# Kernel tuning notes

Hardware: AMD Instinct MI355X
Metric: run time of the kernel (lower is better)

The kernel has to match this reference:

```python
import math
import jax, jax.numpy as jnp
import numpy as np

D_MODEL = 1024
N_HEADS = 16
HEAD_DIM = D_MODEL // N_HEADS  # 64
QDIM = HEAD_DIM // 4           # 16
SPIKE_SLOPE = 5.0
B, S = 2, 2048


def _qweight(r, i, j, k):
    # Hamilton-product weight matrix, identical to QLinear.forward's torch.cat construction.
    return jnp.concatenate([
        jnp.concatenate([r, -i, -j, -k], 1),
        jnp.concatenate([i, r, -k, j], 1),
        jnp.concatenate([j, k, r, -i], 1),
        jnp.concatenate([k, -j, i, r], 1),
    ], 0)


def setup_inputs() -> dict:
    key = jax.random.key(0)
    ks = jax.random.split(key, 20)
    Qo = Qi = D_MODEL // 4  # 256
    p = lambda k, shape, s=0.02: (jax.random.normal(k, shape, dtype=jnp.float32) * s)
    inp = {
        'query': jax.random.normal(ks[0], (B, S, D_MODEL), dtype=jnp.float32),
        'key_in': jax.random.normal(ks[1], (B, S, D_MODEL), dtype=jnp.float32),
        'value': jax.random.normal(ks[2], (B, S, D_MODEL), dtype=jnp.float32),
        'mask': jnp.ones((B, S), dtype=jnp.int32),
        'density_feat': jax.random.normal(ks[3], (B, S, 3), dtype=jnp.float32),
        # q_proj QLinear params
        'wq_r': p(ks[4], (Qo, Qi)), 'wq_i': p(ks[5], (Qo, Qi)),
        'wq_j': p(ks[6], (Qo, Qi)), 'wq_k': p(ks[7], (Qo, Qi)),
        'bq': jnp.zeros((D_MODEL,), jnp.float32),
        # k_proj QLinear params
        'wk_r': p(ks[8], (Qo, Qi)), 'wk_i': p(ks[9], (Qo, Qi)),
        'wk_j': p(ks[10], (Qo, Qi)), 'wk_k': p(ks[11], (Qo, Qi)),
        'bk': jnp.zeros((D_MODEL,), jnp.float32),
        # v_proj / out_proj dense params
        'wv': p(ks[12], (D_MODEL, D_MODEL)), 'bv': jnp.zeros((D_MODEL,), jnp.float32),
        'wo': p(ks[13], (D_MODEL, D_MODEL)), 'bo': jnp.zeros((D_MODEL,), jnp.float32),
        # learned spike threshold (init -1.0 as in torch)
        'threshold': jnp.asarray(-1.0, dtype=jnp.float32),
        # density_mod MLP (use nonzero values so the gate shift is exercised)
        'dm1_w': p(ks[14], (16, 3), 0.5), 'dm1_b': p(ks[15], (16,), 0.1),
        'dm2_w': p(ks[16], (1, 16), 0.5), 'dm2_b': p(ks[17], (1,), 0.1),
    }
    return inp


def reference(query, key_in, value, mask, density_feat,
              wq_r, wq_i, wq_j, wq_k, bq,
              wk_r, wk_i, wk_j, wk_k, bk,
              wv, bv, wo, bo, threshold,
              dm1_w, dm1_b, dm2_w, dm2_b):
    H, hd, Qd = N_HEADS, HEAD_DIM, QDIM
    Bq, Sq, D = query.shape

    Wq = _qweight(wq_r, wq_i, wq_j, wq_k)
    Wk = _qweight(wk_r, wk_i, wk_j, wk_k)
    q = query @ Wq.T + bq
    k = key_in @ Wk.T + bk
    v = value @ wv.T + bv

    # head-major split, matching torch.cat(x.split(hd, -1), dim=0)
    qh = q.reshape(Bq, Sq, H, hd).transpose(2, 0, 1, 3)  # (H,B,S,hd)
    kh = k.reshape(Bq, Sq, H, hd).transpose(2, 0, 1, 3)
    vh = v.reshape(Bq, Sq, H, hd).transpose(2, 0, 1, 3)

    # sum of 4 quaternion-component dot products == full dot product over hd
    scores = jnp.einsum('hbmd,hbnd->hbmn', qh, kh) / math.sqrt(Qd)
    scores = jnp.clip(scores, -6.0, 6.0)

    base_threshold = jax.nn.softplus(threshold)
    h1 = jax.nn.gelu(density_feat @ dm1_w.T + dm1_b, approximate=False)
    d_shift = (h1 @ dm2_w.T + dm2_b)[..., 0]  # (B,N)
    thr = base_threshold + d_shift[None, :, None, :] * 0.1  # (1,B,1,N)

    spike_gate = jax.nn.sigmoid(SPIKE_SLOPE * (scores - thr))
    mod = scores * (1.0 + spike_gate * 2.0)

    m2 = (mask[:, :, None] * mask[:, None, :])[None]  # (1,B,N,N)
    mod = jnp.where(m2 == 0, -10000.0, mod)

    weights = jax.nn.softmax(jnp.clip(mod, -30.0, 30.0), axis=-1)
    # dropout: eval mode (identity)
    out_h = jnp.einsum('hbmn,hbnd->hbmd', weights, vh)
    out = out_h.transpose(1, 2, 0, 3).reshape(Bq, Sq, D)
    return out @ wo.T + bo
```

## Files before the change

kernel.cpp:

```cpp
#include <hip/hip_runtime.h>
#include <stdint.h>
#include <math.h>

#define BB 2
#define SS 2048
#define DM 1024
#define NH 16
#define HD 64
#define MTOT (BB*SS)

typedef __bf16 bf16x8 __attribute__((ext_vector_type(8)));
typedef float  f32x4  __attribute__((ext_vector_type(4)));
typedef float  f32x2  __attribute__((ext_vector_type(2)));
typedef uint32_t u32x4 __attribute__((ext_vector_type(4)));

__device__ __forceinline__ unsigned short f2bf(float f) {
  __bf16 h = (__bf16)f;
  return __builtin_bit_cast(unsigned short, h);
}

__device__ __forceinline__ bf16x8 ldsv8(const unsigned short* p) {
  return __builtin_bit_cast(bf16x8, *(const u32x4*)p);
}

__device__ __forceinline__ void gl16(const void* g, void* l) {
  __builtin_amdgcn_global_load_lds(
      (const __attribute__((address_space(1))) uint32_t*)g,
      (__attribute__((address_space(3))) uint32_t*)l, 16, 0, 0);
}

#define MFMA16(a,b,c) __builtin_amdgcn_mfma_f32_16x16x32_bf16((a),(b),(c),0,0,0)

#define C_NEG5L2E  (-7.213475204444817f)
#define C_L2E      (1.4426950408889634f)
#define C_18L2E    (25.968510736001341f)

__device__ __forceinline__ f32x2 gate_pk(f32x2 s2, float kth, f32x2& lr) {
  s2 = __builtin_elementwise_min(__builtin_elementwise_max(s2, (f32x2){-6.f,-6.f}), (f32x2){6.f,6.f});
  const f32x2 targ = __builtin_elementwise_fma(s2, (f32x2){C_NEG5L2E, C_NEG5L2E}, (f32x2){kth, kth});
  f32x2 t;
  t.x = __builtin_amdgcn_exp2f(targ.x);
  t.y = __builtin_amdgcn_exp2f(targ.y);
  const f32x2 den = t + (f32x2){1.f, 1.f};
  f32x2 g;
  g.x = __builtin_amdgcn_rcpf(den.x);
  g.y = __builtin_amdgcn_rcpf(den.y);
  const f32x2 md = __builtin_elementwise_fma(s2 + s2, g, s2);
  const f32x2 pa = __builtin_elementwise_fma(md, (f32x2){C_L2E, C_L2E}, (f32x2){-C_18L2E, -C_18L2E});
  f32x2 p;
  p.x = __builtin_amdgcn_exp2f(pa.x);
  p.y = __builtin_amdgcn_exp2f(pa.y);
  lr += p;
  return p;
}

__global__ __launch_bounds__(256) void prep_all(
    const float* __restrict__ wqr, const float* __restrict__ wqi,
    const float* __restrict__ wqj, const float* __restrict__ wqk,
    const float* __restrict__ wkr, const float* __restrict__ wki,
    const float* __restrict__ wkj, const float* __restrict__ wkk,
    const float* __restrict__ wv,  const float* __restrict__ wo,
    unsigned short* __restrict__ Wq, unsigned short* __restrict__ Wk,
    unsigned short* __restrict__ Wv, unsigned short* __restrict__ Wo,
    const float* __restrict__ query, const float* __restrict__ key_in,
    const float* __restrict__ value,
    unsigned short* __restrict__ qcv, unsigned short* __restrict__ kcv,
    unsigned short* __restrict__ vcv,
    const float* __restrict__ density, const float* __restrict__ dm1w,
    const float* __restrict__ dm1b, const float* __restrict__ dm2w,
    const float* __restrict__ dm2b, const float* __restrict__ thr_s,
    const int* __restrict__ mask, float2* __restrict__ klim,
    int* __restrict__ amask)
{
  const int bid = blockIdx.x;
  if (bid < 512) {
    const int idx = (bid * 256 + threadIdx.x) * 8;
    const int o = idx >> 10, i = idx & 1023;
    const int br = o >> 8, bc = i >> 8;
    const int ro = o & 255, ci = i & 255;
    const int comp[4][4] = {{0,1,2,3},{1,0,3,2},{2,3,0,1},{3,2,1,0}};
    const float sgn[4][4] = {{1.f,-1.f,-1.f,-1.f},{1.f,1.f,-1.f,1.f},{1.f,1.f,1.f,-1.f},{1.f,-1.f,1.f,1.f}};
    const float* pq[4] = {wqr, wqi, wqj, wqk};
    const float* pk[4] = {wkr, wki, wkj, wkk};
    const int c_ = comp[br][bc];
    const float s_ = sgn[br][bc];
    const float* qsrc = pq[c_] + ro * 256 + ci;
    const float* ksrc = pk[c_] + ro * 256 + ci;
    {
      const float4 f0 = *(const float4*)qsrc;
      const float4 f1 = *(const float4*)(qsrc + 4);
      union { unsigned short us[8]; u32x4 v; } t;
      t.us[0]=f2bf(s_*f0.x); t.us[1]=f2bf(s_*f0.y); t.us[2]=f2bf(s_*f0.z); t.us[3]=f2bf(s_*f0.w);
      t.us[4]=f2bf(s_*f1.x); t.us[5]=f2bf(s_*f1.y); t.us[6]=f2bf(s_*f1.z); t.us[7]=f2bf(s_*f1.w);
      *(u32x4*)(Wq + idx) = t.v;
    }
    {
      const float4 f0 = *(const float4*)ksrc;
      const float4 f1 = *(const float4*)(ksrc + 4);
      union { unsigned short us[8]; u32x4 v; } t;
      t.us[0]=f2bf(s_*f0.x); t.us[1]=f2bf(s_*f0.y); t.us[2]=f2bf(s_*f0.z); t.us[3]=f2bf(s_*f0.w);
      t.us[4]=f2bf(s_*f1.x); t.us[5]=f2bf(s_*f1.y); t.us[6]=f2bf(s_*f1.z); t.us[7]=f2bf(s_*f1.w);
      *(u32x4*)(Wk + idx) = t.v;
    }
    {
      const float4 f0 = *(const float4*)(wv + idx);
      const float4 f1 = *(const float4*)(wv + idx + 4);
      union { unsigned short us[8]; u32x4 v; } t;
      t.us[0]=f2bf(f0.x); t.us[1]=f2bf(f0.y); t.us[2]=f2bf(f0.z); t.us[3]=f2bf(f0.w);
      t.us[4]=f2bf(f1.x); t.us[5]=f2bf(f1.y); t.us[6]=f2bf(f1.z); t.us[7]=f2bf(f1.w);
      *(u32x4*)(Wv + idx) = t.v;
    }
    {
      const float4 f0 = *(const float4*)(wo + idx);
      const float4 f1 = *(const float4*)(wo + idx + 4);
      union { unsigned short us[8]; u32x4 v; } t;
      t.us[0]=f2bf(f0.x); t.us[1]=f2bf(f0.y); t.us[2]=f2bf(f0.z); t.us[3]=f2bf(f0.w);
      t.us[4]=f2bf(f1.x); t.us[5]=f2bf(f1.y); t.us[6]=f2bf(f1.z); t.us[7]=f2bf(f1.w);
      *(u32x4*)(Wo + idx) = t.v;
    }
  } else if (bid < 2560) {
    const int i8 = ((bid - 512) * 256 + threadIdx.x) * 8;
    {
      const float4 f0 = *(const float4*)(query + i8);
      const float4 f1 = *(const float4*)(query + i8 + 4);
      union { unsigned short us[8]; u32x4 v; } t;
      t.us[0]=f2bf(f0.x); t.us[1]=f2bf(f0.y); t.us[2]=f2bf(f0.z); t.us[3]=f2bf(f0.w);
      t.us[4]=f2bf(f1.x); t.us[5]=f2bf(f1.y); t.us[6]=f2bf(f1.z); t.us[7]=f2bf(f1.w);
      *(u32x4*)(qcv + i8) = t.v;
    }
    {
      const float4 f0 = *(const float4*)(key_in + i8);
      const float4 f1 = *(const float4*)(key_in + i8 + 4);
      union { unsigned short us[8]; u32x4 v; } t;
      t.us[0]=f2bf(f0.x); t.us[1]=f2bf(f0.y); t.us[2]=f2bf(f0.z); t.us[3]=f2bf(f0.w);
      t.us[4]=f2bf(f1.x); t.us[5]=f2bf(f1.y); t.us[6]=f2bf(f1.z); t.us[7]=f2bf(f1.w);
      *(u32x4*)(kcv + i8) = t.v;
    }
    {
      const float4 f0 = *(const float4*)(value + i8);
      const float4 f1 = *(const float4*)(value + i8 + 4);
      union { unsigned short us[8]; u32x4 v; } t;
      t.us[0]=f2bf(f0.x); t.us[1]=f2bf(f0.y); t.us[2]=f2bf(f0.z); t.us[3]=f2bf(f0.w);
      t.us[4]=f2bf(f1.x); t.us[5]=f2bf(f1.y); t.us[6]=f2bf(f1.z); t.us[7]=f2bf(f1.w);
      *(u32x4*)(vcv + i8) = t.v;
    }
  } else {
    const int i = (bid - 2560) * 256 + threadIdx.x;
    if (i >= BB * SS) return;
    const float x0 = density[i*3+0], x1 = density[i*3+1], x2 = density[i*3+2];
    const float base = log1pf(expf(thr_s[0]));
    float acc = dm2b[0];
    #pragma unroll
    for (int j = 0; j < 16; ++j) {
      const float hj = dm1w[j*3+0]*x0 + dm1w[j*3+1]*x1 + dm1w[j*3+2]*x2 + dm1b[j];
      const float ge = 0.5f * hj * (1.0f + erff(hj * 0.70710678118654752f));
      acc += dm2w[j] * ge;
    }
    const float thr = base + 0.1f * acc;
    const int mk = mask[i];
    klim[i] = make_float2(thr * (-C_NEG5L2E),
                          mk ? 1e30f : -30.0f);
    const unsigned long long any = __ballot(mk == 0);
    if ((threadIdx.x & 63) == 0 && any)
      atomicOr(&amask[i >> 11], 1);
  }
}

struct GemmArgs {
  const unsigned short* A[3];
  const unsigned short* W[3];
  const float* bias[3];
  void* out[3];
  float scale[3];
  int omode[3];
};

template<int DB>
__global__ __launch_bounds__(256) void gemm_bt(GemmArgs args)
{
  __shared__ __align__(16) unsigned short lA[DB + 1][128*64];
  __shared__ __align__(16) unsigned short lB[DB + 1][128*64];
  const int z = blockIdx.y;
  const int tid = threadIdx.x;
  const int wid = tid >> 6, lane = tid & 63;
  const int l15 = lane & 15, l4 = lane >> 4;
  const int bm = blockIdx.x & 31, bn = blockIdx.x >> 5;
  const int row0 = bm * 128, col0 = bn * 128;
  const int wm = (wid >> 1) * 64, wn = (wid & 1) * 64;

  const unsigned short* gA[4];
  const unsigned short* gB[4];
  #pragma unroll
  for (int i = 0; i < 4; ++i) {
    const int c = (wid * 4 + i) * 64 + lane;
    const int r = c >> 3, jx = c & 7, j = jx ^ (r & 7);
    gA[i] = args.A[z] + (row0 + r) * 1024 + j * 8;
    gB[i] = args.W[z] + (col0 + r) * 1024 + j * 8;
  }

  f32x4 acc[4][4];
  #pragma unroll
  for (int i = 0; i < 4; ++i)
    #pragma unroll
    for (int j = 0; j < 4; ++j) acc[i][j] = (f32x4){0.f,0.f,0.f,0.f};

  #pragma unroll
  for (int i = 0; i < 4; ++i) {
    gl16(gA[i], &lA[0][(wid * 4 + i) * 512]);
    gl16(gB[i], &lB[0][(wid * 4 + i) * 512]);
  }
  if (DB) __syncthreads();

  for (int kt = 0; kt < 16; ++kt) {
    const int cb = DB ? (kt & 1) : 0;
    if (DB) {
      if (kt < 15) {
        const int nb = cb ^ 1, k0 = (kt + 1) * 64;
        #pragma unroll
        for (int i = 0; i < 4; ++i) {
          gl16(gA[i] + k0, &lA[nb][(wid * 4 + i) * 512]);
          gl16(gB[i] + k0, &lB[nb][(wid * 4 + i) * 512]);
        }
      }
    } else {
      if (kt > 0) {
        const int k0 = kt * 64;
        #pragma unroll
        for (int i = 0; i < 4; ++i) {
          gl16(gA[i] + k0, &lA[0][(wid * 4 + i) * 512]);
          gl16(gB[i] + k0, &lB[0][(wid * 4 + i) * 512]);
        }
      }
      __syncthreads();
    }
    #pragma unroll
    for (int kk = 0; kk < 2; ++kk) {
      const int kl = kk * 32 + l4 * 8;
      bf16x8 af[4], bfb[4];
      #pragma unroll
      for (int mi = 0; mi < 4; ++mi) {
        const int r = wm + mi * 16 + l15;
        af[mi] = ldsv8(&lA[cb][r * 64 + (kl ^ ((r & 7) << 3))]);
      }
      #pragma unroll
      for (int nj = 0; nj < 4; ++nj) {
        const int r = wn + nj * 16 + l15;
        bfb[nj] = ldsv8(&lB[cb][r * 64 + (kl ^ ((r & 7) << 3))]);
      }
      #pragma unroll
      for (int mi = 0; mi < 4; ++mi)
        #pragma unroll
        for (int nj = 0; nj < 4; ++nj)
          acc[mi][nj] = MFMA16(af[mi], bfb[nj], acc[mi][nj]);
    }
    __syncthreads();
  }

  const int om = args.omode[z];
  const float sc = args.scale[z];
  void* Cptr = args.out[z];
  #pragma unroll
  for (int nj = 0; nj < 4; ++nj) {
    const int c = col0 + wn + nj * 16 + l15;
    const float bv_ = args.bias[z][c];
    #pragma unroll
    for (int mi = 0; mi < 4; ++mi) {
      const int rb = row0 + wm + mi * 16 + l4 * 4;
      #pragma unroll
      for (int e = 0; e < 4; ++e) {
        const float val = (acc[mi][nj][e] + bv_) * sc;
        const int r = rb + e;
        if (om == 0) {
          ((unsigned short*)Cptr)[r * 1024 + c] = f2bf(val);
        } else if (om == 2) {
          ((float*)Cptr)[r * 1024 + c] = val;
        } else {
          const int h = c >> 6, d = c & 63, b = r >> 11, s = r & 2047;
          ((unsigned short*)Cptr)[((h * BB + b) * HD + d) * SS + s] = f2bf(val);
        }
      }
    }
  }
}

__global__ __launch_bounds__(256, 4) void attn_kernel(
    const unsigned short* __restrict__ qg, const unsigned short* __restrict__ kg,
    const unsigned short* __restrict__ vT, const float2* __restrict__ klim,
    const int* __restrict__ mask, const int* __restrict__ amask,
    unsigned short* __restrict__ outg)
{
  __shared__ __align__(16) unsigned short smem[20480];
  unsigned char* sb = (unsigned char*)smem;
  unsigned short* lK = smem;
  unsigned short* lV = smem + 8192;
  unsigned short* lP = smem + 16384;

  const int tid = threadIdx.x;
  const int wid = tid >> 6, lane = tid & 63;
  const int l15 = lane & 15, l4 = lane >> 4;
  const int rg = wid >> 1, par = wid & 1;
  const int hb = blockIdx.x & 31, qb = blockIdx.x >> 5;
  const int h = hb >> 1, b = hb & 1;
  const int qr0 = qb * 64 + rg * 32;

  const unsigned short* kbase = kg + (b * SS) * DM + h * HD;
  const unsigned short* vbase = vT + ((h * BB + b) * HD) * SS;
  const float2* klimb = klim + b * SS;
  const int clean = (amask[b] == 0);

  const int krho = wid * 8 + (lane >> 3);
  const int kc   = (lane & 7) ^ ((krho >> 1) & 7);
  const unsigned short* ksrc0 = kbase + (size_t)krho * DM + kc * 8;
  const unsigned short* ksrc1 = kbase + (size_t)(32 + krho) * DM + kc * 8;
  const int vd_  = wid * 16 + (lane >> 2);
  const int vc   = (lane & 3) ^ (vd_ & 3);
  const unsigned short* vsrc0 = vbase + (size_t)vd_ * SS + vc * 8;
  const unsigned short* vsrc1 = vbase + (size_t)vd_ * SS + 32 + vc * 8;
  unsigned char* kd0 = sb + wid * 1024;
  unsigned char* kd1 = sb + 4096 + wid * 1024;
  unsigned char* vd0 = sb + 16384 + wid * 1024;
  unsigned char* vd1 = sb + 16384 + 4096 + wid * 1024;

  bf16x8 aq[2][2];
  #pragma unroll
  for (int sr = 0; sr < 2; ++sr) {
    const unsigned short* qs = qg + (b * SS + qr0 + sr * 16 + l15) * DM + h * HD + l4 * 8;
    aq[sr][0] = __builtin_bit_cast(bf16x8, *(const u32x4*)qs);
    aq[sr][1] = __builtin_bit_cast(bf16x8, *(const u32x4*)(qs + 32));
  }
  float limq[2][4];
  if (!clean) {
    #pragma unroll
    for (int sr = 0; sr < 2; ++sr)
      #pragma unroll
      for (int e = 0; e < 4; ++e)
        limq[sr][e] = mask[b * SS + qr0 + sr * 16 + l4 * 4 + e] ? 1e30f : -30.0f;
  }

  f32x2 lr01[2] = {{0.f,0.f},{0.f,0.f}}, lr23[2] = {{0.f,0.f},{0.f,0.f}};
  f32x4 o[2][4];
  #pragma unroll
  for (int sr = 0; sr < 2; ++sr)
    #pragma unroll
    for (int d = 0; d < 4; ++d) o[sr][d] = (f32x4){0.f,0.f,0.f,0.f};

  unsigned short* lPw = lP + wid * 1024;

  gl16(ksrc0, kd0);
  gl16(ksrc1, kd1);
  gl16(vsrc0, vd0);
  gl16(vsrc1, vd1);
  __syncthreads();

  #pragma unroll 2
  for (int pr = 0; pr < 32; ++pr) {
    const int cur = pr & 1;
    const unsigned short* lKt = lK + cur * 4096 + par * 2048;
    const unsigned short* lVt = lV + cur * 4096 + par * 2048;
    const int n0 = pr * 64 + par * 32;

    if (pr < 31) {
      const int co = (cur ^ 1) * 8192;
      const size_t ko = (size_t)(pr + 1) * 64 * DM;
      gl16(ksrc0 + ko, kd0 + co);
      gl16(ksrc1 + ko, kd1 + co);
      gl16(vsrc0 + (pr + 1) * 64, vd0 + co);
      gl16(vsrc1 + (pr + 1) * 64, vd1 + co);
    }

    const float4 klA = *(const float4*)(klimb + n0 + 2 * l15);

    f32x4 sv[2][2];
    __builtin_amdgcn_s_setprio(1);
    #pragma unroll
    for (int cf = 0; cf < 2; ++cf) {
      const int r = 2 * l15 + cf;
      const bf16x8 kf0 = ldsv8(&lKt[r * 64 + ((l4 * 8) ^ ((l15 & 7) << 3))]);
      const bf16x8 kf1 = ldsv8(&lKt[r * 64 + ((32 + l4 * 8) ^ ((l15 & 7) << 3))]);
      #pragma unroll
      for (int sr = 0; sr < 2; ++sr) {
        f32x4 a = (f32x4){0.f,0.f,0.f,0.f};
        a = MFMA16(aq[sr][0], kf0, a);
        a = MFMA16(aq[sr][1], kf1, a);
        sv[sr][cf] = a;
      }
    }
    __builtin_amdgcn_s_setprio(0);

    f32x2 p01[2][2], p23[2][2];
    if (clean) {
      #pragma unroll
      for (int sr = 0; sr < 2; ++sr)
        #pragma unroll
        for (int cf = 0; cf < 2; ++cf) {
          const float kth = cf ? klA.z : klA.x;
          p01[sr][cf] = gate_pk((f32x2){sv[sr][cf][0], sv[sr][cf][1]}, kth, lr01[sr]);
          p23[sr][cf] = gate_pk((f32x2){sv[sr][cf][2], sv[sr][cf][3]}, kth, lr23[sr]);
        }
    } else {
      #pragma unroll
      for (int sr = 0; sr < 2; ++sr)
        #pragma unroll
        for (int cf = 0; cf < 2; ++cf) {
          const float kth = cf ? klA.z : klA.x;
          const float klm = cf ? klA.w : klA.y;
          float pe[4];
          #pragma unroll
          for (int e = 0; e < 4; ++e) {
            float s = fminf(fmaxf(sv[sr][cf][e], -6.f), 6.f);
            const float t = __builtin_amdgcn_exp2f(fmaf(s, C_NEG5L2E, kth));
            const float g = __builtin_amdgcn_rcpf(1.f + t);
            float md = fmaf(s + s, g, s);
            md = fminf(md, fminf(klm, limq[sr][e]));
            pe[e] = __builtin_amdgcn_exp2f(fmaf(md, C_L2E, -C_18L2E));
          }
          p01[sr][cf] = (f32x2){pe[0], pe[1]};
          p23[sr][cf] = (f32x2){pe[2], pe[3]};
          lr01[sr] += p01[sr][cf];
          lr23[sr] += p23[sr][cf];
        }
    }

    #pragma unroll
    for (int sr = 0; sr < 2; ++sr)
      #pragma unroll
      for (int e = 0; e < 4; ++e) {
        const int rr = l4 * 4 + e;
        const float pa_ = (e < 2) ? p01[sr][0][e] : p23[sr][0][e - 2];
        const float pb_ = (e < 2) ? p01[sr][1][e] : p23[sr][1][e - 2];
        union { unsigned short us[2]; unsigned int u; } pk2;
        pk2.us[0] = f2bf(pa_);
        pk2.us[1] = f2bf(pb_);
        *(unsigned int*)&lPw[sr * 512 + rr * 32 + ((2 * l15) ^ ((rr & 3) << 3))] = pk2.u;
      }
    asm volatile("s_waitcnt lgkmcnt(0)" ::: "memory");
    __builtin_amdgcn_sched_barrier(0);

    const bf16x8 pa0 = ldsv8(&lPw[l15 * 32 + ((l4 * 8) ^ ((l15 & 3) << 3))]);
    const bf16x8 pa1 = ldsv8(&lPw[512 + l15 * 32 + ((l4 * 8) ^ ((l15 & 3) << 3))]);

    __builtin_amdgcn_s_setprio(1);
    #pragma unroll
    for (int df = 0; df < 4; ++df) {
      const int d = df * 16 + l15;
      const bf16x8 vf = ldsv8(&lVt[d * 32 + ((l4 * 8) ^ ((d & 3) << 3))]);
      o[0][df] = MFMA16(pa0, vf, o[0][df]);
      o[1][df] = MFMA16(pa1, vf, o[1][df]);
    }
    __builtin_amdgcn_s_setprio(0);

    __syncthreads();
  }

  __syncthreads();
  float* xch = (float*)smem;
  float* slot = xch + rg * 2560;
  if (par) {
    #pragma unroll
    for (int sr = 0; sr < 2; ++sr) {
      #pragma unroll
      for (int df = 0; df < 4; ++df)
        *(f32x4*)&slot[((sr * 4 + df) * 64 + lane) * 4] = o[sr][df];
      f32x4 lr;
      lr[0] = lr01[sr].x; lr[1] = lr01[sr].y; lr[2] = lr23[sr].x; lr[3] = lr23[sr].y;
      *(f32x4*)&slot[2048 + (sr * 64 + lane) * 4] = lr;
    }
  }
  __syncthreads();
  if (!par) {
    #pragma unroll
    for (int sr = 0; sr < 2; ++sr) {
      #pragma unroll
      for (int df = 0; df < 4; ++df) {
        const f32x4 t = *(const f32x4*)&slot[((sr * 4 + df) * 64 + lane) * 4];
        o[sr][df][0] += t[0]; o[sr][df][1] += t[1]; o[sr][df][2] += t[2]; o[sr][df][3] += t[3];
      }
      const f32x4 lrq = *(const f32x4*)&slot[2048 + (sr * 64 + lane) * 4];
      const float lrun[4] = {lr01[sr].x, lr01[sr].y, lr23[sr].x, lr23[sr].y};
      #pragma unroll
      for (int e = 0; e < 4; ++e) {
        float ls = lrun[e] + lrq[e];
        ls += __shfl_xor(ls, 1);
        ls += __shfl_xor(ls, 2);
        ls += __shfl_xor(ls, 4);
        ls += __shfl_xor(ls, 8);
        const float rl = __builtin_amdgcn_rcpf(ls);
        const int r = qr0 + sr * 16 + l4 * 4 + e;
        #pragma unroll
        for (int df = 0; df < 4; ++df) {
          outg[(b * SS + r) * DM + h * HD + df * 16 + l15] = f2bf(o[sr][df][e] * rl);
        }
      }
    }
  }
}

extern "C" void kernel_launch(void* const* d_in, const int* in_sizes, int n_in,
                              void* d_out, int out_size, void* d_ws, size_t ws_size,
                              hipStream_t stream)
{
  const float* query   = (const float*)d_in[0];
  const float* key_in  = (const float*)d_in[1];
  const float* value   = (const float*)d_in[2];
  const int*   mask    = (const int*)d_in[3];
  const float* density = (const float*)d_in[4];
  const float* wq_r = (const float*)d_in[5];
  const float* wq_i = (const float*)d_in[6];
  const float* wq_j = (const float*)d_in[7];
  const float* wq_k = (const float*)d_in[8];
  const float* bq   = (const float*)d_in[9];
  const float* wk_r = (const float*)d_in[10];
  const float* wk_i = (const float*)d_in[11];
  const float* wk_j = (const float*)d_in[12];
  const float* wk_k = (const float*)d_in[13];
  const float* bk   = (const float*)d_in[14];
  const float* wv   = (const float*)d_in[15];
  const float* bv   = (const float*)d_in[16];
  const float* wo   = (const float*)d_in[17];
  const float* bo   = (const float*)d_in[18];
  const float* thrs = (const float*)d_in[19];
  const float* dm1w = (const float*)d_in[20];
  const float* dm1b = (const float*)d_in[21];
  const float* dm2w = (const float*)d_in[22];
  const float* dm2b = (const float*)d_in[23];

  char* ws = (char*)d_ws;
  unsigned short* Wq  = (unsigned short*)(ws + ((size_t)0 << 20));
  unsigned short* Wk  = (unsigned short*)(ws + ((size_t)2 << 20));
  unsigned short* Wv  = (unsigned short*)(ws + ((size_t)4 << 20));
  unsigned short* Wo  = (unsigned short*)(ws + ((size_t)6 << 20));
  unsigned short* qbf = (unsigned short*)(ws + ((size_t)8 << 20));
  unsigned short* kbf = (unsigned short*)(ws + ((size_t)16 << 20));
  unsigned short* vT  = (unsigned short*)(ws + ((size_t)24 << 20));
  unsigned short* att = (unsigned short*)(ws + ((size_t)32 << 20));
  float2* klim        = (float2*)(ws + ((size_t)40 << 20));
  int* amask          = (int*)(ws + ((size_t)40 << 20) + 65536);

  unsigned short* qcv = (unsigned short*)d_out;
  unsigned short* kcv = (unsigned short*)d_out + (size_t)MTOT * DM;
  unsigned short* vcv = att;

  hipMemsetAsync(amask, 0, 2 * sizeof(int), stream);
  prep_all<<<2576, 256, 0, stream>>>(
      wq_r, wq_i, wq_j, wq_k, wk_r, wk_i, wk_j, wk_k, wv, wo,
      Wq, Wk, Wv, Wo,
      query, key_in, value, qcv, kcv, vcv,
      density, dm1w, dm1b, dm2w, dm2b, thrs, mask, klim, amask);

  GemmArgs qkv;
  qkv.A[0] = qcv; qkv.W[0] = Wq; qkv.bias[0] = bq; qkv.out[0] = qbf; qkv.scale[0] = 0.25f; qkv.omode[0] = 0;
  qkv.A[1] = kcv; qkv.W[1] = Wk; qkv.bias[1] = bk; qkv.out[1] = kbf; qkv.scale[1] = 1.0f;  qkv.omode[1] = 0;
  qkv.A[2] = vcv; qkv.W[2] = Wv; qkv.bias[2] = bv; qkv.out[2] = vT;  qkv.scale[2] = 1.0f;  qkv.omode[2] = 1;
  gemm_bt<0><<<dim3(256, 3), 256, 0, stream>>>(qkv);

  attn_kernel<<<1024, 256, 0, stream>>>(qbf, kbf, vT, klim, mask, amask, att);

  GemmArgs og;
  og.A[0] = att; og.W[0] = Wo; og.bias[0] = bo; og.out[0] = d_out; og.scale[0] = 1.0f; og.omode[0] = 2;
  og.A[1] = att; og.W[1] = Wo; og.bias[1] = bo; og.out[1] = d_out; og.scale[1] = 1.0f; og.omode[1] = 2;
  og.A[2] = att; og.W[2] = Wo; og.bias[2] = bo; og.out[2] = d_out; og.scale[2] = 1.0f; og.omode[2] = 2;
  gemm_bt<1><<<dim3(256, 1), 256, 0, stream>>>(og);
}
```

Before: 176.6 us.

## Double attention block to 128 query rows with 512 threads sharing K/V tiles

Attention blocks grow from 4 to 8 waves, each covering 128 query rows instead of 64. This halves the number of blocks, so every K/V tile loaded into LDS serves twice as many query rows. Each wave now issues one K and one V async load per iteration instead of two. LDS per block grows to hold more P scratch, and fewer, larger blocks may lower occupancy and make the barrier-synchronised pipeline coarser.

Measured after the change: 402.2 us. 128% more time.

```diff
diff --git a/kernel.cpp b/kernel.cpp
--- a/kernel.cpp
+++ b/kernel.cpp
@@ -283,13 +283,13 @@
   }
 }
 
-__global__ __launch_bounds__(256, 4) void attn_kernel(
+__global__ __launch_bounds__(512, 6) void attn_kernel(
     const unsigned short* __restrict__ qg, const unsigned short* __restrict__ kg,
     const unsigned short* __restrict__ vT, const float2* __restrict__ klim,
     const int* __restrict__ mask, const int* __restrict__ amask,
     unsigned short* __restrict__ outg)
 {
-  __shared__ __align__(16) unsigned short smem[20480];
+  __shared__ __align__(16) unsigned short smem[24576];
   unsigned char* sb = (unsigned char*)smem;
   unsigned short* lK = smem;
   unsigned short* lV = smem + 8192;
@@ -301,25 +301,22 @@
   const int rg = wid >> 1, par = wid & 1;
   const int hb = blockIdx.x & 31, qb = blockIdx.x >> 5;
   const int h = hb >> 1, b = hb & 1;
-  const int qr0 = qb * 64 + rg * 32;
+  const int qr0 = qb * 128 + rg * 32;
 
   const unsigned short* kbase = kg + (b * SS) * DM + h * HD;
   const unsigned short* vbase = vT + ((h * BB + b) * HD) * SS;
   const float2* klimb = klim + b * SS;
   const int clean = (amask[b] == 0);
 
-  const int krho = wid * 8 + (lane >> 3);
+  const int sp  = wid >> 2, ci = wid & 3;
+  const int krho = ci * 8 + (lane >> 3);
   const int kc   = (lane & 7) ^ ((krho >> 1) & 7);
-  const unsigned short* ksrc0 = kbase + (size_t)krho * DM + kc * 8;
-  const unsigned short* ksrc1 = kbase + (size_t)(32 + krho) * DM + kc * 8;
-  const int vd_  = wid * 16 + (lane >> 2);
+  const unsigned short* ksrc = kbase + (size_t)(sp * 32 + krho) * DM + kc * 8;
+  const int vd_  = ci * 16 + (lane >> 2);
   const int vc   = (lane & 3) ^ (vd_ & 3);
-  const unsigned short* vsrc0 = vbase + (size_t)vd_ * SS + vc * 8;
-  const unsigned short* vsrc1 = vbase + (size_t)vd_ * SS + 32 + vc * 8;
-  unsigned char* kd0 = sb + wid * 1024;
-  unsigned char* kd1 = sb + 4096 + wid * 1024;
-  unsigned char* vd0 = sb + 16384 + wid * 1024;
-  unsigned char* vd1 = sb + 16384 + 4096 + wid * 1024;
+  const unsigned short* vsrc = vbase + (size_t)vd_ * SS + sp * 32 + vc * 8;
+  unsigned char* kdw = sb + sp * 4096 + ci * 1024;
+  unsigned char* vdw = sb + 16384 + sp * 4096 + ci * 1024;
 
   bf16x8 aq[2][2];
   #pragma unroll
@@ -346,10 +343,8 @@
 
   unsigned short* lPw = lP + wid * 1024;
 
-  gl16(ksrc0, kd0);
-  gl16(ksrc1, kd1);
-  gl16(vsrc0, vd0);
-  gl16(vsrc1, vd1);
+  gl16(ksrc, kdw);
+  gl16(vsrc, vdw);
   __syncthreads();
 
   #pragma unroll 2
@@ -361,11 +356,8 @@
 
     if (pr < 31) {
       const int co = (cur ^ 1) * 8192;
-      const size_t ko = (size_t)(pr + 1) * 64 * DM;
-      gl16(ksrc0 + ko, kd0 + co);
-      gl16(ksrc1 + ko, kd1 + co);
-      gl16(vsrc0 + (pr + 1) * 64, vd0 + co);
-      gl16(vsrc1 + (pr + 1) * 64, vd1 + co);
+      gl16(ksrc + (size_t)(pr + 1) * 64 * DM, kdw + co);
+      gl16(vsrc + (pr + 1) * 64,              vdw + co);
     }
 
     const float4 klA = *(const float4*)(klimb + n0 + 2 * l15);
@@ -553,7 +545,7 @@
   qkv.A[2] = vcv; qkv.W[2] = Wv; qkv.bias[2] = bv; qkv.out[2] = vT;  qkv.scale[2] = 1.0f;  qkv.omode[2] = 1;
   gemm_bt<0><<<dim3(256, 3), 256, 0, stream>>>(qkv);
 
-  attn_kernel<<<1024, 256, 0, stream>>>(qbf, kbf, vT, klim, mask, amask, att);
+  attn_kernel<<<512, 512, 0, stream>>>(qbf, kbf, vT, klim, mask, amask, att);
 
   GemmArgs og;
   og.A[0] = att; og.W[0] = Wo; og.bias[0] = bo; og.out[0] = d_out; og.scale[0] = 1.0f; og.omode[0] = 2;
```
